# Optimization experiments

Hardware: AMD Instinct MI355X
Metric: run time of the kernel (lower is better)

The kernel has to match this reference:

```python
import jax, jax.numpy as jnp
import numpy as np

EPS = 1e-12  # keras K.l2_normalize epsilon


def setup_inputs() -> dict:
    key = jax.random.key(0)
    k1, k2, k3 = jax.random.split(key, 3)
    B, T, C = 4, 4096, 64
    L = 15
    N_NODE = 64
    x = jax.random.normal(k1, (B, T, C), dtype=jnp.float32)
    w = jax.random.normal(k2, (L,), dtype=jnp.float32)            # st_conv_filter_one
    conv_w = jax.random.normal(k3, (C * C, N_NODE), dtype=jnp.float32) * 0.02  # 1x1 conv kernel
    conv_b = jnp.zeros((N_NODE,), dtype=jnp.float32)
    return {"x": x, "w": w, "conv_w": conv_w, "conv_b": conv_b}


def reference(x, w, conv_w, conv_b):
    B, T, C = x.shape
    L = w.shape[0]
    pad = L // 2
    # ZeroPadding1D(local_size//2): pad time axis on both sides
    x_pad = jnp.pad(x, ((0, 0), (pad, pad), (0, 0)))  # [B, T+2*pad, C]
    # Gather sliding windows: [B, T, L, C]
    idx = jnp.arange(T)[:, None] + jnp.arange(L)[None, :]
    xw = x_pad[:, idx, :]
    # Bilinear form per frame: X^T diag(w) X -> [B, T, C, C]
    bil = jnp.einsum('btlc,l,btld->btcd', xw, w, xw)
    # Flatten to [B, T, C*C]
    feat = bil.reshape(B, T, C * C)
    # L2 normalize along last axis (keras K.l2_normalize)
    sq = jnp.sum(feat * feat, axis=-1, keepdims=True)
    feat = feat * jax.lax.rsqrt(jnp.maximum(sq, EPS))
    # 1x1 Conv1D(n_node) == per-frame dense layer
    out = jnp.einsum('btk,kn->btn', feat, conv_w) + conv_b
    return out
```

## Files before the change

### kernel.cpp

```cpp
#include <hip/hip_runtime.h>
#include <stdint.h>

#define T_DIM 4096
#define S_DIM 16384
#define EPSF 1e-12f

typedef __attribute__((ext_vector_type(8))) short   short8v;
typedef __attribute__((ext_vector_type(4))) float   float4v;
typedef __attribute__((ext_vector_type(4))) uint32_t uint4v;

__device__ __forceinline__ unsigned short f2bf_rne(float f) {
    uint32_t u = __builtin_bit_cast(uint32_t, f);
    return (unsigned short)((u + 0x7fffu + ((u >> 16) & 1u)) >> 16);
}
__device__ __forceinline__ uint32_t cvtpk(float lo, float hi) {
    uint32_t r;
    asm("v_cvt_pk_bf16_f32 %0, %1, %2" : "=v"(r) : "v"(lo), "v"(hi));
    return r;
}

__global__ __launch_bounds__(256) void k_convert(const float* __restrict__ conv_w,
                                                 unsigned short* __restrict__ wfrag) {
    __shared__ unsigned short lb[64][65];
    int tid = threadIdx.x;
    int cc  = blockIdx.x;
    for (int i = tid; i < 4096; i += 256) {
        lb[i >> 6][i & 63] = f2bf_rne(conv_w[((size_t)cc << 12) + i]);
    }
    __syncthreads();
    for (int gi = tid; gi < 512; gi += 256) {
        int nt = gi >> 7, h = (gi >> 6) & 1, ln = gi & 63;
        int n  = (nt << 4) + (ln & 15);
        int kb = (h << 5) + ((ln >> 4) << 3);
        uint4v u;
        #pragma unroll
        for (int q = 0; q < 4; ++q)
            u[q] = (uint32_t)lb[kb + 2 * q][n] | ((uint32_t)lb[kb + 2 * q + 1][n] << 16);
        *(uint4v*)(wfrag + ((size_t)cc << 12) + (gi << 3)) = u;
    }
}

__global__ __launch_bounds__(256) void k_dotsP(const float* __restrict__ x,
                                               const float* __restrict__ w,
                                               float* __restrict__ P) {
    __shared__ float xt[78 * 65];
    __shared__ float pd[4][64][17];
    __shared__ float dsq[64][17];
    int tid = threadIdx.x, lane = tid & 63, wv = tid >> 6;
    int s0 = blockIdx.x << 6;
    int bt0 = s0 & (T_DIM - 1);
    for (int i = tid; i < 78 * 16; i += 256) {
        int r = i >> 4, c4 = (i & 15) << 2;
        float4v v = {0.f, 0.f, 0.f, 0.f};
        if (bt0 + r < T_DIM) v = *(const float4v*)(x + (((size_t)(s0 + r)) << 6) + c4);
        #pragma unroll
        for (int q = 0; q < 4; ++q) xt[r * 65 + c4 + q] = v[q];
    }
    __syncthreads();
    float acc[15];
    #pragma unroll
    for (int j = 0; j < 15; ++j) acc[j] = 0.f;
    int c0 = wv << 4;
    for (int c = c0; c < c0 + 16; ++c) {
        const float* base = &xt[lane * 65 + c];
        float xl = base[0];
        #pragma unroll
        for (int j = 0; j < 15; ++j) acc[j] += xl * base[j * 65];
    }
    #pragma unroll
    for (int j = 0; j < 15; ++j) pd[wv][lane][j] = acc[j];
    __syncthreads();
    for (int i = tid; i < 960; i += 256) {
        int s = i & 63, j = i >> 6;
        float d = pd[0][s][j] + pd[1][s][j] + pd[2][s][j] + pd[3][s][j];
        dsq[s][j] = d * d;
    }
    __syncthreads();
    for (int i = tid; i < 960; i += 256) {
        int s = i & 63, l = i >> 6;
        float sum = w[l] * dsq[s][0];
        for (int j = 1; j <= 14 - l; ++j) sum += 2.f * w[l + j] * dsq[s][j];
        P[(size_t)l * S_DIM + s0 + s] = sum;
    }
}

__global__ __launch_bounds__(256) void k_rsq(const float* __restrict__ P,
                                             const float* __restrict__ w,
                                             float* __restrict__ rsq) {
    int s = blockIdx.x * 256 + threadIdx.x;
    int t = s & (T_DIM - 1);
    float sum = 0.f;
    #pragma unroll
    for (int l = 0; l < 15; ++l) {
        int tp = t + l - 7;
        if (0 <= tp && tp < T_DIM) sum += w[l] * P[(size_t)l * S_DIM + s + l - 7];
    }
    rsq[s] = rsqrtf(fmaxf(sum, EPSF));
}

__global__ __launch_bounds__(256) void k_gemm(const float* __restrict__ x,
                                              const unsigned short* __restrict__ wfrag,
                                              float* __restrict__ g) {
    int tid = threadIdx.x, lane = tid & 63, wv = tid >> 6;
    int split = blockIdx.x & 3;
    int m0 = (blockIdx.x >> 2) << 6;
    int c0 = split << 4;

    int prow = (wv << 4) + (lane & 15);
    int kgrp = (lane >> 4) << 3;
    const float* xr = x + (((size_t)(m0 + prow)) << 6);
    float4v p00 = *(const float4v*)(xr + kgrp);
    float4v p01 = *(const float4v*)(xr + kgrp + 4);
    float4v p10 = *(const float4v*)(xr + 32 + kgrp);
    float4v p11 = *(const float4v*)(xr + 36 + kgrp);

    const short8v* wf = (const short8v*)wfrag;

    float4v acc[4];
    #pragma unroll
    for (int nt = 0; nt < 4; ++nt)
        #pragma unroll
        for (int j = 0; j < 4; ++j) acc[nt][j] = 0.f;

    #pragma unroll 2
    for (int ci = 0; ci < 16; ++ci) {
        const short8v* base = wf + (((size_t)(c0 + ci)) << 9) + lane;
        short8v b0 = base[0];
        short8v b1 = base[64];
        short8v b2 = base[128];
        short8v b3 = base[192];
        short8v b4 = base[256];
        short8v b5 = base[320];
        short8v b6 = base[384];
        short8v b7 = base[448];

        float xc = xr[c0 + ci];
        union { uint32_t u[4]; short8v s; } a0, a1;
        float4v q0 = p00 * xc, q1 = p01 * xc, q2 = p10 * xc, q3 = p11 * xc;
        a0.u[0] = cvtpk(q0[0], q0[1]); a0.u[1] = cvtpk(q0[2], q0[3]);
        a0.u[2] = cvtpk(q1[0], q1[1]); a0.u[3] = cvtpk(q1[2], q1[3]);
        a1.u[0] = cvtpk(q2[0], q2[1]); a1.u[1] = cvtpk(q2[2], q2[3]);
        a1.u[2] = cvtpk(q3[0], q3[1]); a1.u[3] = cvtpk(q3[2], q3[3]);

        acc[0] = __builtin_amdgcn_mfma_f32_16x16x32_bf16(a0.s, b0, acc[0], 0, 0, 0);
        acc[0] = __builtin_amdgcn_mfma_f32_16x16x32_bf16(a1.s, b1, acc[0], 0, 0, 0);
        acc[1] = __builtin_amdgcn_mfma_f32_16x16x32_bf16(a0.s, b2, acc[1], 0, 0, 0);
        acc[1] = __builtin_amdgcn_mfma_f32_16x16x32_bf16(a1.s, b3, acc[1], 0, 0, 0);
        acc[2] = __builtin_amdgcn_mfma_f32_16x16x32_bf16(a0.s, b4, acc[2], 0, 0, 0);
        acc[2] = __builtin_amdgcn_mfma_f32_16x16x32_bf16(a1.s, b5, acc[2], 0, 0, 0);
        acc[3] = __builtin_amdgcn_mfma_f32_16x16x32_bf16(a0.s, b6, acc[3], 0, 0, 0);
        acc[3] = __builtin_amdgcn_mfma_f32_16x16x32_bf16(a1.s, b7, acc[3], 0, 0, 0);
    }

    float* gp = g + (size_t)split * ((size_t)S_DIM * 64);
    int crow0 = m0 + (wv << 4) + ((lane >> 4) << 2);
    int col0 = lane & 15;
    #pragma unroll
    for (int nt = 0; nt < 4; ++nt)
        #pragma unroll
        for (int j = 0; j < 4; ++j)
            gp[((size_t)(crow0 + j) << 6) + (nt << 4) + col0] = acc[nt][j];
}

__global__ __launch_bounds__(256) void k_final(const float* __restrict__ g,
                                               const float* __restrict__ rsq,
                                               const float* __restrict__ w,
                                               const float* __restrict__ conv_b,
                                               float* __restrict__ out) {
    int lane = threadIdx.x & 63, wv = threadIdx.x >> 6;
    int wid = blockIdx.x * 4 + wv;
    int t0 = wid << 4;
    int bt0 = t0 & (T_DIM - 1);
    const size_t SP = (size_t)S_DIM * 64;
    float r[30];
    #pragma unroll
    for (int i = 0; i < 30; ++i) {
        int tr = bt0 - 7 + i;
        r[i] = 0.f;
        if (0 <= tr && tr < T_DIM) {
            const float* p = g + (((size_t)(t0 - 7 + i)) << 6) + lane;
            r[i] = (p[0] + p[SP]) + (p[2 * SP] + p[3 * SP]);
        }
    }
    float bn = conv_b[lane];
    #pragma unroll
    for (int i = 0; i < 16; ++i) {
        float acc = 0.f;
        #pragma unroll
        for (int l = 0; l < 15; ++l) acc += w[l] * r[i + l];
        out[(((size_t)(t0 + i)) << 6) + lane] = acc * rsq[t0 + i] + bn;
    }
}

extern "C" void kernel_launch(void* const* d_in, const int* in_sizes, int n_in,
                              void* d_out, int out_size, void* d_ws, size_t ws_size,
                              hipStream_t stream) {
    const float* x      = (const float*)d_in[0];
    const float* w      = (const float*)d_in[1];
    const float* conv_w = (const float*)d_in[2];
    const float* conv_b = (const float*)d_in[3];
    float* out = (float*)d_out;

    char* ws = (char*)d_ws;
    unsigned short* wfrag = (unsigned short*)ws;
    float* g              = (float*)(ws + 524288);
    float* P              = (float*)(ws + 524288 + 16777216);
    float* rsq            = P + (size_t)15 * S_DIM;

    hipLaunchKernelGGL(k_convert, dim3(64),   dim3(256), 0, stream, conv_w, wfrag);
    hipLaunchKernelGGL(k_dotsP,   dim3(256),  dim3(256), 0, stream, x, w, P);
    hipLaunchKernelGGL(k_gemm,    dim3(1024), dim3(256), 0, stream, x, wfrag, g);
    hipLaunchKernelGGL(k_rsq,     dim3(64),   dim3(256), 0, stream, P, w, rsq);
    hipLaunchKernelGGL(k_final,   dim3(256),  dim3(256), 0, stream, g, rsq, w, conv_b, out);
}
```

Measured before the change: 61.28 us.

## Factor outer-product GEMM: MFMA on raw x rows, scale by x_c afterward

The GEMM kernel no longer forms x_c*x_d products in the A operand for every c. It converts the x row to bf16 once, runs MFMA with the per-c weight slab, and then scales each output row by x_c in fp32 and accumulates. The warp decomposition also changes: each wave now owns one 16-column output tile across all 64 rows instead of 16 rows across all columns. This removes the per-iteration multiply and convert work and halves weight loads per wave. In exchange it adds scalar x loads and FMA accumulation after each MFMA, and the rounding behaviour changes (x is rounded to bf16 rather than the product).

```diff
diff --git a/kernel.cpp b/kernel.cpp
--- a/kernel.cpp
+++ b/kernel.cpp
@@ -7,6 +7,7 @@
 
 typedef __attribute__((ext_vector_type(8))) short   short8v;
 typedef __attribute__((ext_vector_type(4))) float   float4v;
+typedef __attribute__((ext_vector_type(2))) float   float2v;
 typedef __attribute__((ext_vector_type(4))) uint32_t uint4v;
 
 __device__ __forceinline__ unsigned short f2bf_rne(float f) {
@@ -106,60 +107,67 @@
     int m0 = (blockIdx.x >> 2) << 6;
     int c0 = split << 4;
 
-    int prow = (wv << 4) + (lane & 15);
-    int kgrp = (lane >> 4) << 3;
-    const float* xr = x + (((size_t)(m0 + prow)) << 6);
-    float4v p00 = *(const float4v*)(xr + kgrp);
-    float4v p01 = *(const float4v*)(xr + kgrp + 4);
-    float4v p10 = *(const float4v*)(xr + 32 + kgrp);
-    float4v p11 = *(const float4v*)(xr + 36 + kgrp);
-
-    const short8v* wf = (const short8v*)wfrag;
+    int arow_l = lane & 15;
+    int kgrp   = (lane >> 4) << 3;
+    int srow_b = (lane >> 4) << 2;
+
+    short8v xd[4][2];
+    #pragma unroll
+    for (int rg = 0; rg < 4; ++rg) {
+        const float* xr = x + (((size_t)(m0 + rg * 16 + arow_l)) << 6);
+        #pragma unroll
+        for (int h = 0; h < 2; ++h) {
+            float4v v0 = *(const float4v*)(xr + h * 32 + kgrp);
+            float4v v1 = *(const float4v*)(xr + h * 32 + kgrp + 4);
+            union { uint32_t u[4]; short8v s; } a;
+            a.u[0] = cvtpk(v0[0], v0[1]); a.u[1] = cvtpk(v0[2], v0[3]);
+            a.u[2] = cvtpk(v1[0], v1[1]); a.u[3] = cvtpk(v1[2], v1[3]);
+            xd[rg][h] = a.s;
+        }
+    }
 
     float4v acc[4];
     #pragma unroll
-    for (int nt = 0; nt < 4; ++nt)
-        #pragma unroll
-        for (int j = 0; j < 4; ++j) acc[nt][j] = 0.f;
-
-    #pragma unroll 2
-    for (int ci = 0; ci < 16; ++ci) {
-        const short8v* base = wf + (((size_t)(c0 + ci)) << 9) + lane;
-        short8v b0 = base[0];
-        short8v b1 = base[64];
-        short8v b2 = base[128];
-        short8v b3 = base[192];
-        short8v b4 = base[256];
-        short8v b5 = base[320];
-        short8v b6 = base[384];
-        short8v b7 = base[448];
-
-        float xc = xr[c0 + ci];
-        union { uint32_t u[4]; short8v s; } a0, a1;
-        float4v q0 = p00 * xc, q1 = p01 * xc, q2 = p10 * xc, q3 = p11 * xc;
-        a0.u[0] = cvtpk(q0[0], q0[1]); a0.u[1] = cvtpk(q0[2], q0[3]);
-        a0.u[2] = cvtpk(q1[0], q1[1]); a0.u[3] = cvtpk(q1[2], q1[3]);
-        a1.u[0] = cvtpk(q2[0], q2[1]); a1.u[1] = cvtpk(q2[2], q2[3]);
-        a1.u[2] = cvtpk(q3[0], q3[1]); a1.u[3] = cvtpk(q3[2], q3[3]);
-
-        acc[0] = __builtin_amdgcn_mfma_f32_16x16x32_bf16(a0.s, b0, acc[0], 0, 0, 0);
-        acc[0] = __builtin_amdgcn_mfma_f32_16x16x32_bf16(a1.s, b1, acc[0], 0, 0, 0);
-        acc[1] = __builtin_amdgcn_mfma_f32_16x16x32_bf16(a0.s, b2, acc[1], 0, 0, 0);
-        acc[1] = __builtin_amdgcn_mfma_f32_16x16x32_bf16(a1.s, b3, acc[1], 0, 0, 0);
-        acc[2] = __builtin_amdgcn_mfma_f32_16x16x32_bf16(a0.s, b4, acc[2], 0, 0, 0);
-        acc[2] = __builtin_amdgcn_mfma_f32_16x16x32_bf16(a1.s, b5, acc[2], 0, 0, 0);
-        acc[3] = __builtin_amdgcn_mfma_f32_16x16x32_bf16(a0.s, b6, acc[3], 0, 0, 0);
-        acc[3] = __builtin_amdgcn_mfma_f32_16x16x32_bf16(a1.s, b7, acc[3], 0, 0, 0);
+    for (int rg = 0; rg < 4; ++rg)
+        #pragma unroll
+        for (int j = 0; j < 4; ++j) acc[rg][j] = 0.f;
+
+    const short8v* wfb = (const short8v*)wfrag + ((size_t)wv << 7) + lane;
+
+    #pragma unroll 1
+    for (int cg = 0; cg < 8; ++cg) {
+        int cbase = c0 + (cg << 1);
+        float2v xs[4][4];
+        #pragma unroll
+        for (int rg = 0; rg < 4; ++rg)
+            #pragma unroll
+            for (int j = 0; j < 4; ++j)
+                xs[rg][j] = *(const float2v*)(
+                    x + (((size_t)(m0 + rg * 16 + srow_b + j)) << 6) + cbase);
+        #pragma unroll
+        for (int cc = 0; cc < 2; ++cc) {
+            const short8v* bp = wfb + (((size_t)(cbase + cc)) << 9);
+            short8v b0 = bp[0];
+            short8v b1 = bp[64];
+            #pragma unroll
+            for (int rg = 0; rg < 4; ++rg) {
+                float4v hh = {0.f, 0.f, 0.f, 0.f};
+                hh = __builtin_amdgcn_mfma_f32_16x16x32_bf16(xd[rg][0], b0, hh, 0, 0, 0);
+                hh = __builtin_amdgcn_mfma_f32_16x16x32_bf16(xd[rg][1], b1, hh, 0, 0, 0);
+                #pragma unroll
+                for (int j = 0; j < 4; ++j)
+                    acc[rg][j] += xs[rg][j][cc] * hh[j];
+            }
+        }
     }
 
     float* gp = g + (size_t)split * ((size_t)S_DIM * 64);
-    int crow0 = m0 + (wv << 4) + ((lane >> 4) << 2);
-    int col0 = lane & 15;
-    #pragma unroll
-    for (int nt = 0; nt < 4; ++nt)
+    int col = (wv << 4) + arow_l;
+    #pragma unroll
+    for (int rg = 0; rg < 4; ++rg)
         #pragma unroll
         for (int j = 0; j < 4; ++j)
-            gp[((size_t)(crow0 + j) << 6) + (nt << 4) + col0] = acc[nt][j];
+            gp[((size_t)(m0 + rg * 16 + srow_b + j) << 6) + col] = acc[rg][j];
 }
 
 __global__ __launch_bounds__(256) void k_final(const float* __restrict__ g,
```

Result: slower. 66.11 us (+7.9%).

## Stage GEMM weight fragments through double-buffered LDS with async global-to-LDS loads

Applied to the files above, without the earlier changes.

The GEMM kernel used to have all four waves load the same 8 KB weight fragment chunk per channel straight from global memory. It now copies each chunk once per block into a double-buffered LDS array using global_load_lds, prefetching the next chunk while MFMAs run on the current one. This cuts redundant global and L2 traffic by about 4x but adds a block-wide barrier every iteration and extra LDS reads. Correctness depends on the global_load_lds writes being visible after __syncthreads, meaning the vmcnt wait must be honored.

```diff
diff --git a/kernel.cpp b/kernel.cpp
--- a/kernel.cpp
+++ b/kernel.cpp
@@ -18,6 +18,11 @@
     asm("v_cvt_pk_bf16_f32 %0, %1, %2" : "=v"(r) : "v"(lo), "v"(hi));
     return r;
 }
+
+#define GLOAD_LDS16(gsrc, ldst)                                                     \
+    __builtin_amdgcn_global_load_lds(                                               \
+        (const __attribute__((address_space(1))) void*)(gsrc),                      \
+        (__attribute__((address_space(3))) void*)(ldst), 16, 0, 0)
 
 __global__ __launch_bounds__(256) void k_convert(const float* __restrict__ conv_w,
                                                  unsigned short* __restrict__ wfrag) {
@@ -101,6 +106,7 @@
 __global__ __launch_bounds__(256) void k_gemm(const float* __restrict__ x,
                                               const unsigned short* __restrict__ wfrag,
                                               float* __restrict__ g) {
+    __shared__ alignas(16) unsigned short wbuf[2][4096];
     int tid = threadIdx.x, lane = tid & 63, wv = tid >> 6;
     int split = blockIdx.x & 3;
     int m0 = (blockIdx.x >> 2) << 6;
@@ -114,25 +120,39 @@
     float4v p10 = *(const float4v*)(xr + 32 + kgrp);
     float4v p11 = *(const float4v*)(xr + 36 + kgrp);
 
-    const short8v* wf = (const short8v*)wfrag;
+    const char* wsb = (const char*)wfrag;
+#define STAGE_CHUNK(bi, c) do {                                                   \
+        GLOAD_LDS16(wsb + ((size_t)(c) << 13) + (tid << 4),                       \
+                    (char*)&wbuf[bi][0] + (wv << 10));                            \
+        GLOAD_LDS16(wsb + ((size_t)(c) << 13) + 4096 + (tid << 4),                \
+                    (char*)&wbuf[bi][0] + 4096 + (wv << 10));                     \
+    } while (0)
 
     float4v acc[4];
     #pragma unroll
     for (int nt = 0; nt < 4; ++nt)
         #pragma unroll
         for (int j = 0; j < 4; ++j) acc[nt][j] = 0.f;
+
+    const short8v* fb0 = (const short8v*)&wbuf[0][0];
+    const short8v* fb1 = (const short8v*)&wbuf[1][0];
+
+    STAGE_CHUNK(0, c0);
+    __syncthreads();
 
     #pragma unroll 2
     for (int ci = 0; ci < 16; ++ci) {
-        const short8v* base = wf + (((size_t)(c0 + ci)) << 9) + lane;
-        short8v b0 = base[0];
-        short8v b1 = base[64];
-        short8v b2 = base[128];
-        short8v b3 = base[192];
-        short8v b4 = base[256];
-        short8v b5 = base[320];
-        short8v b6 = base[384];
-        short8v b7 = base[448];
+        if (ci < 15) STAGE_CHUNK((ci + 1) & 1, c0 + ci + 1);
+
+        const short8v* fb = (ci & 1) ? fb1 : fb0;
+        short8v b0 = fb[lane];
+        short8v b1 = fb[64 + lane];
+        short8v b2 = fb[128 + lane];
+        short8v b3 = fb[192 + lane];
+        short8v b4 = fb[256 + lane];
+        short8v b5 = fb[320 + lane];
+        short8v b6 = fb[384 + lane];
+        short8v b7 = fb[448 + lane];
 
         float xc = xr[c0 + ci];
         union { uint32_t u[4]; short8v s; } a0, a1;
@@ -150,7 +170,10 @@
         acc[2] = __builtin_amdgcn_mfma_f32_16x16x32_bf16(a1.s, b5, acc[2], 0, 0, 0);
         acc[3] = __builtin_amdgcn_mfma_f32_16x16x32_bf16(a0.s, b6, acc[3], 0, 0, 0);
         acc[3] = __builtin_amdgcn_mfma_f32_16x16x32_bf16(a1.s, b7, acc[3], 0, 0, 0);
-    }
+
+        __syncthreads();
+    }
+#undef STAGE_CHUNK
 
     float* gp = g + (size_t)split * ((size_t)S_DIM * 64);
     int crow0 = m0 + (wv << 4) + ((lane >> 4) << 2);
```

Measured after the change: 52.09 us, median of 2. 15.0% less time.
